# Performance work log

Measured on AMD Instinct MI355X. Metric: run time of the kernel, lower is better.

Reference implementation:

```python
import jax, jax.numpy as jnp
import numpy as np

B, S, D = 2, 2048, 2048
H = 16
HD = D // H
DFF = 4 * D
EPS = 1e-5


def _layernorm(x, g, b):
    mu = jnp.mean(x, axis=-1, keepdims=True)
    var = jnp.mean(jnp.square(x - mu), axis=-1, keepdims=True)
    return (x - mu) * jax.lax.rsqrt(var + EPS) * g + b


def setup_inputs() -> dict:
    key = jax.random.key(0)
    ks = jax.random.split(key, 12)
    s_d = 1.0 / np.sqrt(D)
    s_ff = 1.0 / np.sqrt(DFF)
    return {
        "x": jax.random.normal(ks[0], (B, S, D), dtype=jnp.float32),
        "attention_mask": jnp.ones((B, S), dtype=jnp.int32),
        "ln1_g": jnp.ones((D,), jnp.float32),
        "ln1_b": jnp.zeros((D,), jnp.float32),
        "wq": jax.random.uniform(ks[1], (D, D), jnp.float32, -s_d, s_d),
        "bq": jnp.zeros((D,), jnp.float32),
        "wk": jax.random.uniform(ks[2], (D, D), jnp.float32, -s_d, s_d),
        "bk": jnp.zeros((D,), jnp.float32),
        "wv": jax.random.uniform(ks[3], (D, D), jnp.float32, -s_d, s_d),
        "bv": jnp.zeros((D,), jnp.float32),
        "wo": jax.random.uniform(ks[4], (D, D), jnp.float32, -s_d, s_d),
        "bo": jnp.zeros((D,), jnp.float32),
        "ln2_g": jnp.ones((D,), jnp.float32),
        "ln2_b": jnp.zeros((D,), jnp.float32),
        "w1": jax.random.uniform(ks[5], (D, DFF), jnp.float32, -s_d, s_d),
        "b1": jnp.zeros((DFF,), jnp.float32),
        "w2": jax.random.uniform(ks[6], (DFF, D), jnp.float32, -s_ff, s_ff),
        "b2": jnp.zeros((D,), jnp.float32),
    }


def reference(x, attention_mask, ln1_g, ln1_b, wq, bq, wk, bk, wv, bv, wo, bo,
              ln2_g, ln2_b, w1, b1, w2, b2):
    # ---- attention (pre-LN) ----
    h = _layernorm(x, ln1_g, ln1_b)  # [B,S,D]
    q = (h @ wq + bq).reshape(B, S, H, HD).transpose(0, 2, 1, 3)  # [B,H,S,HD]
    k = (h @ wk + bk).reshape(B, S, H, HD).transpose(0, 2, 1, 3)
    v = (h @ wv + bv).reshape(B, S, H, HD).transpose(0, 2, 1, 3)
    scores = jnp.einsum('bhqd,bhkd->bhqk', q, k) / np.sqrt(HD)  # [B,H,S,S]
    causal = jnp.tril(jnp.ones((S, S), dtype=bool))
    neg_inf = jnp.float32(-jnp.inf)
    scores = jnp.where(causal[None, None], scores, neg_inf)
    pad = (attention_mask != 0)[:, None, None, :]  # [B,1,1,S] over keys
    scores = jnp.where(pad, scores, neg_inf)
    w = jax.nn.softmax(scores, axis=-1)
    attn = jnp.einsum('bhqk,bhkd->bhqd', w, v)  # [B,H,S,HD]
    attn = attn.transpose(0, 2, 1, 3).reshape(B, S, D)
    x = x + (attn @ wo + bo)
    # ---- FFN (pre-LN) ----
    h2 = _layernorm(x, ln2_g, ln2_b)
    ff = jax.nn.gelu(h2 @ w1 + b1, approximate=False) @ w2 + b2
    return x + ff
```

## Files before the change

kernel.cpp:

```cpp
#include <hip/hip_runtime.h>
#include <cmath>

#define BB 2
#define SS 2048
#define DD 2048
#define HH 16
#define HDIM 128
#define DFF 8192
#define MROWS 4096

typedef unsigned short u16;
typedef unsigned int u32;
typedef short short8 __attribute__((ext_vector_type(8)));
typedef u16 u16x8 __attribute__((ext_vector_type(8)));
typedef float f32x4 __attribute__((ext_vector_type(4)));
typedef float f4 __attribute__((ext_vector_type(4)));

__device__ __forceinline__ u16 f2bf(float f) {
  u32 u = __float_as_uint(f);
  u = (u + 0x7fffu + ((u >> 16) & 1u)) >> 16;
  return (u16)u;
}

__device__ __forceinline__ f32x4 mfma16(short8 a, short8 b, f32x4 c) {
  return __builtin_amdgcn_mfma_f32_16x16x32_bf16(a, b, c, 0, 0, 0);
}

__device__ __forceinline__ void gload16(const void* g, void* l) {
  __builtin_amdgcn_global_load_lds((const __attribute__((address_space(1))) u32*)g,
                                   (__attribute__((address_space(3))) u32*)l, 16, 0, 0);
}

__global__ __launch_bounds__(256) void transpose_w(const float* __restrict__ W,
                                                   u16* __restrict__ Wt, int K, int N) {
  __shared__ float t[32][33];
  int n0 = blockIdx.x * 32, k0 = blockIdx.y * 32;
  int tx = threadIdx.x & 31, ty = threadIdx.x >> 5;
#pragma unroll
  for (int i = 0; i < 4; i++) t[ty + i * 8][tx] = W[(size_t)(k0 + ty + i * 8) * N + n0 + tx];
  __syncthreads();
#pragma unroll
  for (int i = 0; i < 4; i++)
    Wt[(size_t)(n0 + ty + i * 8) * K + k0 + tx] = f2bf(t[tx][ty + i * 8]);
}

__global__ void prep_mask(const int* __restrict__ m, float* __restrict__ kb) {
  int i = blockIdx.x * 256 + threadIdx.x;
  kb[i] = m[i] ? 0.f : -1e30f;
}

__global__ __launch_bounds__(256) void ln_bf16(const float* __restrict__ x,
                                               const float* __restrict__ g,
                                               const float* __restrict__ bta,
                                               u16* __restrict__ out) {
  int row = blockIdx.x;
  int t = threadIdx.x;
  const f4* xr = (const f4*)(x + (size_t)row * DD);
  f4 a = xr[t * 2], c = xr[t * 2 + 1];
  float s = a[0] + a[1] + a[2] + a[3] + c[0] + c[1] + c[2] + c[3];
  float q = a[0]*a[0] + a[1]*a[1] + a[2]*a[2] + a[3]*a[3]
          + c[0]*c[0] + c[1]*c[1] + c[2]*c[2] + c[3]*c[3];
#pragma unroll
  for (int off = 32; off >= 1; off >>= 1) {
    s += __shfl_down(s, off);
    q += __shfl_down(q, off);
  }
  __shared__ float red[8];
  int wv = t >> 6;
  if ((t & 63) == 0) { red[wv] = s; red[4 + wv] = q; }
  __syncthreads();
  s = red[0] + red[1] + red[2] + red[3];
  q = red[4] + red[5] + red[6] + red[7];
  float mu = s * (1.f / DD);
  float rstd = rsqrtf(q * (1.f / DD) - mu * mu + 1e-5f);
  const f4* gp = (const f4*)g;
  const f4* bp = (const f4*)bta;
  f4 g0 = gp[t * 2], g1 = gp[t * 2 + 1], b0 = bp[t * 2], b1 = bp[t * 2 + 1];
  u16x8 r8;
  r8[0] = f2bf((a[0] - mu) * rstd * g0[0] + b0[0]);
  r8[1] = f2bf((a[1] - mu) * rstd * g0[1] + b0[1]);
  r8[2] = f2bf((a[2] - mu) * rstd * g0[2] + b0[2]);
  r8[3] = f2bf((a[3] - mu) * rstd * g0[3] + b0[3]);
  r8[4] = f2bf((c[0] - mu) * rstd * g1[0] + b1[0]);
  r8[5] = f2bf((c[1] - mu) * rstd * g1[1] + b1[1]);
  r8[6] = f2bf((c[2] - mu) * rstd * g1[2] + b1[2]);
  r8[7] = f2bf((c[3] - mu) * rstd * g1[3] + b1[7-4]);
  *(u16x8*)(out + (size_t)row * DD + t * 8) = r8;
}

template <int EPI>
__global__ __launch_bounds__(256, 4) void gemm_bt(const u16* __restrict__ A,
                                               const u16* __restrict__ Bt,
                                               const float* __restrict__ bias,
                                               const float* __restrict__ bias2,
                                               const float* __restrict__ bias3,
                                               const float* __restrict__ resid,
                                               void* __restrict__ outp,
                                               int M, int N, int K, float scale) {
  __shared__ u16 As[128 * 32];
  __shared__ u16 Bs[128 * 32];
  int tid = threadIdx.x, w = tid >> 6, lane = tid & 63, ln = lane & 15, quad = lane >> 4;
  int n0 = blockIdx.x * 128, m0 = blockIdx.y * 128;
  int wm = (w & 1) * 64, wn = (w >> 1) * 64;
  f32x4 acc[4][4] = {};
  const u16* ap = A + (size_t)m0 * K;
  const u16* bp = Bt + (size_t)n0 * K;
  int nkt = K >> 5;
  for (int kt = 0; kt < nkt; kt++) {
    int k0 = kt * 32;
#pragma unroll
    for (int i = 0; i < 2; i++) {
      int c = i * 256 + tid, row = c >> 2, cc = c & 3;
      gload16(ap + (size_t)row * K + k0 + cc * 8, &As[c * 8]);
    }
#pragma unroll
    for (int i = 0; i < 2; i++) {
      int c = i * 256 + tid, row = c >> 2, cc = c & 3;
      gload16(bp + (size_t)row * K + k0 + cc * 8, &Bs[c * 8]);
    }
    __syncthreads();
    short8 af[4], bf[4];
#pragma unroll
    for (int i = 0; i < 4; i++) af[i] = *(const short8*)&As[(wm + i * 16 + ln) * 32 + quad * 8];
#pragma unroll
    for (int j = 0; j < 4; j++) bf[j] = *(const short8*)&Bs[(wn + j * 16 + ln) * 32 + quad * 8];
#pragma unroll
    for (int i = 0; i < 4; i++)
#pragma unroll
      for (int j = 0; j < 4; j++) acc[i][j] = mfma16(af[i], bf[j], acc[i][j]);
    __syncthreads();
  }
#pragma unroll
  for (int i = 0; i < 4; i++) {
    int row = m0 + wm + i * 16 + quad * 4;
#pragma unroll
    for (int j = 0; j < 4; j++) {
      int col = n0 + wn + j * 16 + ln;
      float bvv;
      int qkv = 0, dcol = col;
      if (EPI == 4) {
        qkv = col >> 11;
        dcol = col & 2047;
        bvv = (qkv == 0 ? bias : qkv == 1 ? bias2 : bias3)[dcol];
      } else {
        bvv = bias[col];
      }
#pragma unroll
      for (int r = 0; r < 4; r++) {
        float v = acc[i][j][r] + bvv;
        int rw = row + r;
        if (EPI == 2) {
          v += resid[(size_t)rw * N + col];
          ((float*)outp)[(size_t)rw * N + col] = v;
        } else if (EPI == 3) {
          float gv = 0.5f * v * (1.0f + erff(v * 0.70710678118654752f));
          ((u16*)outp)[(size_t)rw * N + col] = f2bf(gv);
        } else {
          int b_ = rw >> 11, s_ = rw & 2047, hh = dcol >> 7, hd = dcol & 127;
          u16* o16 = (u16*)outp;
          if (qkv == 0) {
            o16[(((size_t)(b_ * HH + hh) * SS + s_) << 7) + hd] = f2bf(v * scale);
          } else if (qkv == 1) {
            o16[8388608 + (((size_t)(b_ * HH + hh) * SS + s_) << 7) + hd] = f2bf(v);
          } else {
            o16[16777216 + (((size_t)(b_ * HH + hh) * HDIM + hd) << 11) + s_] = f2bf(v);
          }
        }
      }
    }
  }
}

__global__ __launch_bounds__(256, 4) void gemm_bt_splitk(const u16* __restrict__ A,
                                                      const u16* __restrict__ Bt,
                                                      float* __restrict__ P,
                                                      int M, int N, int K, int klen) {
  __shared__ u16 As[128 * 32];
  __shared__ u16 Bs[128 * 32];
  int tid = threadIdx.x, w = tid >> 6, lane = tid & 63, ln = lane & 15, quad = lane >> 4;
  int n0 = blockIdx.x * 128, m0 = blockIdx.y * 128, z = blockIdx.z;
  int kbeg = z * klen;
  int wm = (w & 1) * 64, wn = (w >> 1) * 64;
  f32x4 acc[4][4] = {};
  const u16* ap = A + (size_t)m0 * K + kbeg;
  const u16* bp = Bt + (size_t)n0 * K + kbeg;
  float* Pz = P + (size_t)z * M * N;
  int nkt = klen >> 5;
  for (int kt = 0; kt < nkt; kt++) {
    int k0 = kt * 32;
#pragma unroll
    for (int i = 0; i < 2; i++) {
      int c = i * 256 + tid, row = c >> 2, cc = c & 3;
      gload16(ap + (size_t)row * K + k0 + cc * 8, &As[c * 8]);
    }
#pragma unroll
    for (int i = 0; i < 2; i++) {
      int c = i * 256 + tid, row = c >> 2, cc = c & 3;
      gload16(bp + (size_t)row * K + k0 + cc * 8, &Bs[c * 8]);
    }
    __syncthreads();
    short8 af[4], bf[4];
#pragma unroll
    for (int i = 0; i < 4; i++) af[i] = *(const short8*)&As[(wm + i * 16 + ln) * 32 + quad * 8];
#pragma unroll
    for (int j = 0; j < 4; j++) bf[j] = *(const short8*)&Bs[(wn + j * 16 + ln) * 32 + quad * 8];
#pragma unroll
    for (int i = 0; i < 4; i++)
#pragma unroll
      for (int j = 0; j < 4; j++) acc[i][j] = mfma16(af[i], bf[j], acc[i][j]);
    __syncthreads();
  }
#pragma unroll
  for (int i = 0; i < 4; i++) {
    int row = m0 + wm + i * 16 + quad * 4;
#pragma unroll
    for (int j = 0; j < 4; j++) {
      int col = n0 + wn + j * 16 + ln;
#pragma unroll
      for (int r = 0; r < 4; r++) Pz[(size_t)(row + r) * N + col] = acc[i][j][r];
    }
  }
}

__global__ __launch_bounds__(256) void splitk_fix(const float* __restrict__ P0,
                                                  const float* __restrict__ P1,
                                                  const float* __restrict__ bias,
                                                  const float* __restrict__ resid,
                                                  float* __restrict__ out) {
  int i = blockIdx.x * 1024 + threadIdx.x * 4;
  f4 a = *(const f4*)(P0 + i);
  f4 b = *(const f4*)(P1 + i);
  f4 rr = *(const f4*)(resid + i);
  f4 bb = *(const f4*)(bias + (i & 2047));
  f4 o = a + b + rr + bb;
  *(f4*)(out + i) = o;
}

__global__ __launch_bounds__(256) void attn_kernel(const u16* __restrict__ Q,
                                                   const u16* __restrict__ Kg,
                                                   const u16* __restrict__ Vtg,
                                                   const float* __restrict__ kb,
                                                   u16* __restrict__ Out) {
  __shared__ u16 Ks[2][64 * 128];
  __shared__ u16 Vs[2][128 * 64];
  __shared__ u16 Ps[64 * 64];
  int tid = threadIdx.x, w = tid >> 6, lane = tid & 63, ln = lane & 15, quad = lane >> 4;
  int bh = blockIdx.y, b = bh >> 4;
  const u16* kgB = Kg + (size_t)bh * SS * HDIM;
  const u16* vgB = Vtg + (size_t)bh * HDIM * SS;

  auto stage = [&](int buf, int kt) {
    const u16* kg = kgB + (size_t)kt * 64 * HDIM;
#pragma unroll
    for (int i = 0; i < 4; i++) {
      int c = i * 256 + tid, r = c >> 4;
      int jl = (c & 15) ^ (r & 7);
      gload16(kg + r * HDIM + jl * 8, &Ks[buf][c * 8]);
    }
    const u16* vg = vgB + kt * 64;
#pragma unroll
    for (int i = 0; i < 4; i++) {
      int c = i * 256 + tid, r = c >> 3;
      int jl = (c & 7) ^ (r & 7);
      gload16(vg + (size_t)r * SS + jl * 8, &Vs[buf][c * 8]);
    }
  };

#pragma unroll 1
  for (int half = 0; half < 2; half++) {
    int qt = half ? (31 - blockIdx.x) : blockIdx.x;
    int q0 = qt * 64;
    short8 qf[4];
    size_t qbase = ((size_t)bh * SS + q0 + w * 16 + ln) * HDIM;
#pragma unroll
    for (int ks = 0; ks < 4; ks++) qf[ks] = *(const short8*)(Q + qbase + ks * 32 + quad * 8);
    f32x4 o[8] = {};
    float mrow[4], lrow[4];
#pragma unroll
    for (int r = 0; r < 4; r++) { mrow[r] = -1e30f; lrow[r] = 0.f; }
    int nkt = qt + 1;
    __syncthreads();
    stage(0, 0);
    int cur = 0;
    for (int kt = 0; kt < nkt; kt++) {
      __syncthreads();
      if (kt + 1 < nkt) stage(cur ^ 1, kt + 1);
      const u16* KsB = Ks[cur];
      const u16* VsB = Vs[cur];
      float kbv[4];
#pragma unroll
      for (int nt = 0; nt < 4; nt++) kbv[nt] = kb[b * SS + kt * 64 + nt * 16 + ln];
      f32x4 sc[4] = {};
#pragma unroll
      for (int ks = 0; ks < 4; ks++)
#pragma unroll
        for (int nt = 0; nt < 4; nt++) {
          short8 kf = *(const short8*)&KsB[(nt * 16 + ln) * 128 +
                                           (((ks * 4 + quad) ^ (ln & 7)) << 3)];
          sc[nt] = mfma16(qf[ks], kf, sc[nt]);
        }
      bool diag = (kt == nkt - 1);
      int rowg = q0 + w * 16 + quad * 4;
      float mt[4] = {-3e30f, -3e30f, -3e30f, -3e30f};
#pragma unroll
      for (int nt = 0; nt < 4; nt++) {
        int colg = kt * 64 + nt * 16 + ln;
#pragma unroll
        for (int r = 0; r < 4; r++) {
          float s = sc[nt][r] + kbv[nt];
          if (diag && colg > rowg + r) s = -3e30f;
          sc[nt][r] = s;
          mt[r] = fmaxf(mt[r], s);
        }
      }
#pragma unroll
      for (int off = 8; off >= 1; off >>= 1)
#pragma unroll
        for (int r = 0; r < 4; r++) mt[r] = fmaxf(mt[r], __shfl_xor(mt[r], off, 16));
      float al[4], lt[4];
#pragma unroll
      for (int r = 0; r < 4; r++) {
        float mn = fmaxf(mrow[r], mt[r]);
        al[r] = __expf(mrow[r] - mn);
        mrow[r] = mn;
        lt[r] = 0.f;
      }
#pragma unroll
      for (int nt = 0; nt < 4; nt++)
#pragma unroll
        for (int r = 0; r < 4; r++) {
          float e = __expf(sc[nt][r] - mrow[r]);
          sc[nt][r] = e;
          lt[r] += e;
        }
#pragma unroll
      for (int off = 8; off >= 1; off >>= 1)
#pragma unroll
        for (int r = 0; r < 4; r++) lt[r] += __shfl_xor(lt[r], off, 16);
#pragma unroll
      for (int r = 0; r < 4; r++) lrow[r] = lrow[r] * al[r] + lt[r];
#pragma unroll
      for (int h8 = 0; h8 < 8; h8++)
#pragma unroll
        for (int r = 0; r < 4; r++) o[h8][r] *= al[r];
#pragma unroll
      for (int nt = 0; nt < 4; nt++)
#pragma unroll
        for (int r = 0; r < 4; r++) {
          int prow = w * 16 + quad * 4 + r;
          int pcol = nt * 16 + ln;
          Ps[prow * 64 + (((pcol >> 3) ^ (prow & 7)) << 3) + (pcol & 7)] = f2bf(sc[nt][r]);
        }
#pragma unroll
      for (int ks2 = 0; ks2 < 2; ks2++) {
        int sw = ((ks2 * 4 + quad) ^ (ln & 7)) << 3;
        short8 pf = *(const short8*)&Ps[(w * 16 + ln) * 64 + sw];
#pragma unroll
        for (int h8 = 0; h8 < 8; h8++) {
          short8 vf = *(const short8*)&VsB[(h8 * 16 + ln) * 64 + sw];
          o[h8] = mfma16(pf, vf, o[h8]);
        }
      }
      cur ^= 1;
    }
    float inv[4];
#pragma unroll
    for (int r = 0; r < 4; r++) inv[r] = 1.0f / lrow[r];
    int srow = q0 + w * 16 + quad * 4;
#pragma unroll
    for (int h8 = 0; h8 < 8; h8++) {
      int col = h8 * 16 + ln;
#pragma unroll
      for (int r = 0; r < 4; r++) {
        size_t idx = ((size_t)b * SS + srow + r) * DD + (size_t)(bh & 15) * HDIM + col;
        Out[idx] = f2bf(o[h8][r] * inv[r]);
      }
    }
  }
}

extern "C" void kernel_launch(void* const* d_in, const int* in_sizes, int n_in,
                              void* d_out, int out_size, void* d_ws, size_t ws_size,
                              hipStream_t stream) {
  const float* x    = (const float*)d_in[0];
  const int*   amask= (const int*)d_in[1];
  const float* ln1g = (const float*)d_in[2];
  const float* ln1b = (const float*)d_in[3];
  const float* wq   = (const float*)d_in[4];
  const float* bq   = (const float*)d_in[5];
  const float* wk   = (const float*)d_in[6];
  const float* bk   = (const float*)d_in[7];
  const float* wv   = (const float*)d_in[8];
  const float* bv   = (const float*)d_in[9];
  const float* wo   = (const float*)d_in[10];
  const float* bo   = (const float*)d_in[11];
  const float* ln2g = (const float*)d_in[12];
  const float* ln2b = (const float*)d_in[13];
  const float* w1   = (const float*)d_in[14];
  const float* b1   = (const float*)d_in[15];
  const float* w2   = (const float*)d_in[16];
  const float* b2   = (const float*)d_in[17];

  char* ws = (char*)d_ws;
  u16* wqT  = (u16*)(ws + 0);
  u16* wkT  = (u16*)(ws + 8388608);
  u16* wvT  = (u16*)(ws + 16777216);
  u16* woT  = (u16*)(ws + 25165824);
  u16* w1T  = (u16*)(ws + 33554432);
  u16* w2T  = (u16*)(ws + 67108864);
  u16* hbuf = (u16*)(ws + 100663296);
  u16* qbuf = (u16*)(ws + 117440512);
  u16* kbuf = (u16*)(ws + 134217728);
  u16* vtb  = (u16*)(ws + 150994944);
  u16* atb  = (u16*)(ws + 167772160);
  float* x2 = (float*)(ws + 184549376);
  float* kb = (float*)(ws + 218103808);
  u16* ff1  = qbuf;
  float* pbuf = (float*)(ws + 0);

  transpose_w<<<dim3(64, 64), 256, 0, stream>>>(wq, wqT, 2048, 2048);
  transpose_w<<<dim3(64, 64), 256, 0, stream>>>(wk, wkT, 2048, 2048);
  transpose_w<<<dim3(64, 64), 256, 0, stream>>>(wv, wvT, 2048, 2048);
  transpose_w<<<dim3(64, 64), 256, 0, stream>>>(wo, woT, 2048, 2048);
  transpose_w<<<dim3(256, 64), 256, 0, stream>>>(w1, w1T, 2048, 8192);
  transpose_w<<<dim3(64, 256), 256, 0, stream>>>(w2, w2T, 8192, 2048);
  prep_mask<<<16, 256, 0, stream>>>(amask, kb);

  ln_bf16<<<4096, 256, 0, stream>>>(x, ln1g, ln1b, hbuf);
  const float qscale = 0.08838834764831845f;
  gemm_bt<4><<<dim3(48, 32), 256, 0, stream>>>(hbuf, wqT, bq, bk, bv, nullptr, qbuf,
                                               4096, 6144, 2048, qscale);
  attn_kernel<<<dim3(16, 32), 256, 0, stream>>>(qbuf, kbuf, vtb, kb, atb);
  gemm_bt<2><<<dim3(16, 32), 256, 0, stream>>>(atb, woT, bo, nullptr, nullptr, x, x2,
                                               4096, 2048, 2048, 1.0f);

  ln_bf16<<<4096, 256, 0, stream>>>(x2, ln2g, ln2b, hbuf);
  gemm_bt<3><<<dim3(64, 32), 256, 0, stream>>>(hbuf, w1T, b1, nullptr, nullptr, nullptr, ff1,
                                               4096, 8192, 2048, 1.0f);
  gemm_bt_splitk<<<dim3(16, 32, 2), 256, 0, stream>>>(ff1, w2T, pbuf, 4096, 2048, 8192, 4096);
  splitk_fix<<<8192, 256, 0, stream>>>(pbuf, pbuf + (size_t)4096 * 2048, b2, x2,
                                       (float*)d_out);
}
```

Baseline: 937.9 us.

## Double GEMM K-tile to 64 with XOR-swizzled LDS layout; vectorize weight transpose stores

Both GEMM kernels now stage 64-wide K tiles instead of 32, halving the number of barrier pairs per output tile. An XOR swizzle on the 16-byte chunk index, applied consistently to the global-to-LDS loads and the LDS fragment reads, is meant to avoid bank conflicts in the wider rows. The weight transpose now writes four bf16 values per thread as one vector store. LDS per block doubles to 32 KB, which may limit occupancy under launch_bounds(256,4).

```diff
diff --git a/kernel.cpp b/kernel.cpp
--- a/kernel.cpp
+++ b/kernel.cpp
@@ -12,6 +12,7 @@
 typedef unsigned short u16;
 typedef unsigned int u32;
 typedef short short8 __attribute__((ext_vector_type(8)));
+typedef u16 u16x4 __attribute__((ext_vector_type(4)));
 typedef u16 u16x8 __attribute__((ext_vector_type(8)));
 typedef float f32x4 __attribute__((ext_vector_type(4)));
 typedef float f4 __attribute__((ext_vector_type(4)));
@@ -39,9 +40,11 @@
 #pragma unroll
   for (int i = 0; i < 4; i++) t[ty + i * 8][tx] = W[(size_t)(k0 + ty + i * 8) * N + n0 + tx];
   __syncthreads();
-#pragma unroll
-  for (int i = 0; i < 4; i++)
-    Wt[(size_t)(n0 + ty + i * 8) * K + k0 + tx] = f2bf(t[tx][ty + i * 8]);
+  int n = threadIdx.x >> 3, kq = threadIdx.x & 7;
+  u16x4 v;
+#pragma unroll
+  for (int m = 0; m < 4; m++) v[m] = f2bf(t[kq * 4 + m][n]);
+  *(u16x4*)&Wt[(size_t)(n0 + n) * K + k0 + kq * 4] = v;
 }
 
 __global__ void prep_mask(const int* __restrict__ m, float* __restrict__ kb) {
@@ -84,7 +87,7 @@
   r8[4] = f2bf((c[0] - mu) * rstd * g1[0] + b1[0]);
   r8[5] = f2bf((c[1] - mu) * rstd * g1[1] + b1[1]);
   r8[6] = f2bf((c[2] - mu) * rstd * g1[2] + b1[2]);
-  r8[7] = f2bf((c[3] - mu) * rstd * g1[3] + b1[7-4]);
+  r8[7] = f2bf((c[3] - mu) * rstd * g1[3] + b1[3]);
   *(u16x8*)(out + (size_t)row * DD + t * 8) = r8;
 }
 
@@ -97,37 +100,42 @@
                                                const float* __restrict__ resid,
                                                void* __restrict__ outp,
                                                int M, int N, int K, float scale) {
-  __shared__ u16 As[128 * 32];
-  __shared__ u16 Bs[128 * 32];
+  __shared__ u16 As[128 * 64];
+  __shared__ u16 Bs[128 * 64];
   int tid = threadIdx.x, w = tid >> 6, lane = tid & 63, ln = lane & 15, quad = lane >> 4;
   int n0 = blockIdx.x * 128, m0 = blockIdx.y * 128;
   int wm = (w & 1) * 64, wn = (w >> 1) * 64;
   f32x4 acc[4][4] = {};
   const u16* ap = A + (size_t)m0 * K;
   const u16* bp = Bt + (size_t)n0 * K;
-  int nkt = K >> 5;
+  int nkt = K >> 6;
   for (int kt = 0; kt < nkt; kt++) {
-    int k0 = kt * 32;
-#pragma unroll
-    for (int i = 0; i < 2; i++) {
-      int c = i * 256 + tid, row = c >> 2, cc = c & 3;
-      gload16(ap + (size_t)row * K + k0 + cc * 8, &As[c * 8]);
-    }
-#pragma unroll
-    for (int i = 0; i < 2; i++) {
-      int c = i * 256 + tid, row = c >> 2, cc = c & 3;
-      gload16(bp + (size_t)row * K + k0 + cc * 8, &Bs[c * 8]);
+    int k0 = kt * 64;
+#pragma unroll
+    for (int i = 0; i < 4; i++) {
+      int c = i * 256 + tid, row = c >> 3, sl = c & 7;
+      gload16(ap + (size_t)row * K + k0 + ((sl ^ (row & 7)) << 3), &As[c * 8]);
+    }
+#pragma unroll
+    for (int i = 0; i < 4; i++) {
+      int c = i * 256 + tid, row = c >> 3, sl = c & 7;
+      gload16(bp + (size_t)row * K + k0 + ((sl ^ (row & 7)) << 3), &Bs[c * 8]);
     }
     __syncthreads();
-    short8 af[4], bf[4];
-#pragma unroll
-    for (int i = 0; i < 4; i++) af[i] = *(const short8*)&As[(wm + i * 16 + ln) * 32 + quad * 8];
-#pragma unroll
-    for (int j = 0; j < 4; j++) bf[j] = *(const short8*)&Bs[(wn + j * 16 + ln) * 32 + quad * 8];
-#pragma unroll
-    for (int i = 0; i < 4; i++)
-#pragma unroll
-      for (int j = 0; j < 4; j++) acc[i][j] = mfma16(af[i], bf[j], acc[i][j]);
+#pragma unroll
+    for (int h = 0; h < 2; h++) {
+      short8 af[4], bf[4];
+#pragma unroll
+      for (int i = 0; i < 4; i++)
+        af[i] = *(const short8*)&As[(wm + i * 16 + ln) * 64 + (((h * 4 + quad) ^ (ln & 7)) << 3)];
+#pragma unroll
+      for (int j = 0; j < 4; j++)
+        bf[j] = *(const short8*)&Bs[(wn + j * 16 + ln) * 64 + (((h * 4 + quad) ^ (ln & 7)) << 3)];
+#pragma unroll
+      for (int i = 0; i < 4; i++)
+#pragma unroll
+        for (int j = 0; j < 4; j++) acc[i][j] = mfma16(af[i], bf[j], acc[i][j]);
+    }
     __syncthreads();
   }
 #pragma unroll
@@ -175,8 +183,8 @@
                                                       const u16* __restrict__ Bt,
                                                       float* __restrict__ P,
                                                       int M, int N, int K, int klen) {
-  __shared__ u16 As[128 * 32];
-  __shared__ u16 Bs[128 * 32];
+  __shared__ u16 As[128 * 64];
+  __shared__ u16 Bs[128 * 64];
   int tid = threadIdx.x, w = tid >> 6, lane = tid & 63, ln = lane & 15, quad = lane >> 4;
   int n0 = blockIdx.x * 128, m0 = blockIdx.y * 128, z = blockIdx.z;
   int kbeg = z * klen;
@@ -185,29 +193,34 @@
   const u16* ap = A + (size_t)m0 * K + kbeg;
   const u16* bp = Bt + (size_t)n0 * K + kbeg;
   float* Pz = P + (size_t)z * M * N;
-  int nkt = klen >> 5;
+  int nkt = klen >> 6;
   for (int kt = 0; kt < nkt; kt++) {
-    int k0 = kt * 32;
-#pragma unroll
-    for (int i = 0; i < 2; i++) {
-      int c = i * 256 + tid, row = c >> 2, cc = c & 3;
-      gload16(ap + (size_t)row * K + k0 + cc * 8, &As[c * 8]);
-    }
-#pragma unroll
-    for (int i = 0; i < 2; i++) {
-      int c = i * 256 + tid, row = c >> 2, cc = c & 3;
-      gload16(bp + (size_t)row * K + k0 + cc * 8, &Bs[c * 8]);
+    int k0 = kt * 64;
+#pragma unroll
+    for (int i = 0; i < 4; i++) {
+      int c = i * 256 + tid, row = c >> 3, sl = c & 7;
+      gload16(ap + (size_t)row * K + k0 + ((sl ^ (row & 7)) << 3), &As[c * 8]);
+    }
+#pragma unroll
+    for (int i = 0; i < 4; i++) {
+      int c = i * 256 + tid, row = c >> 3, sl = c & 7;
+      gload16(bp + (size_t)row * K + k0 + ((sl ^ (row & 7)) << 3), &Bs[c * 8]);
     }
     __syncthreads();
-    short8 af[4], bf[4];
-#pragma unroll
-    for (int i = 0; i < 4; i++) af[i] = *(const short8*)&As[(wm + i * 16 + ln) * 32 + quad * 8];
-#pragma unroll
-    for (int j = 0; j < 4; j++) bf[j] = *(const short8*)&Bs[(wn + j * 16 + ln) * 32 + quad * 8];
-#pragma unroll
-    for (int i = 0; i < 4; i++)
-#pragma unroll
-      for (int j = 0; j < 4; j++) acc[i][j] = mfma16(af[i], bf[j], acc[i][j]);
+#pragma unroll
+    for (int h = 0; h < 2; h++) {
+      short8 af[4], bf[4];
+#pragma unroll
+      for (int i = 0; i < 4; i++)
+        af[i] = *(const short8*)&As[(wm + i * 16 + ln) * 64 + (((h * 4 + quad) ^ (ln & 7)) << 3)];
+#pragma unroll
+      for (int j = 0; j < 4; j++)
+        bf[j] = *(const short8*)&Bs[(wn + j * 16 + ln) * 64 + (((h * 4 + quad) ^ (ln & 7)) << 3)];
+#pragma unroll
+      for (int i = 0; i < 4; i++)
+#pragma unroll
+        for (int j = 0; j < 4; j++) acc[i][j] = mfma16(af[i], bf[j], acc[i][j]);
+    }
     __syncthreads();
   }
 #pragma unroll
```

Measured after the change: 853.8 us. -9.0%, faster.
